# Kernel optimization log

Measured on AMD Instinct MI355X. Metric: run time of the kernel, lower is better.

Reference implementation:

```python
import jax, jax.numpy as jnp
import numpy as np

E = 8       # num_experts
TOP_K = 2
H = 512     # hidden_size
DFF = 2048  # expert FFN inner dim (4*H)
B, S = 4, 2048


def setup_inputs() -> dict:
    key = jax.random.key(0)
    k0, k1, k2, k3 = jax.random.split(key, 4)
    return {
        "hidden_states": jax.random.normal(k0, (B, S, H), jnp.float32),
        # router gate: kaiming-ish init scaled by 0.01 (near-uniform routing)
        "gate_w": jax.random.normal(k1, (E, H), jnp.float32) * 0.01,
        "w1": jax.random.normal(k2, (E, H, DFF), jnp.float32) * (1.0 / np.sqrt(H)),
        "b1": jnp.zeros((E, DFF), jnp.float32),
        "w2": jax.random.normal(k3, (E, DFF, H), jnp.float32) * (1.0 / np.sqrt(DFF)),
        "b2": jnp.zeros((E, H), jnp.float32),
    }


def reference(hidden_states, gate_w, w1, b1, w2, b2):
    # hidden_states: (B, S, H)
    b, s, h = hidden_states.shape
    flat = hidden_states.reshape(-1, h)                 # (T, H), T = B*S

    # --- TopKRouter (eval mode: no gaussian noise) ---
    logits = flat @ gate_w.T                            # (T, E)
    top_vals, top_idx = jax.lax.top_k(logits, TOP_K)    # (T, K)
    top_w = jax.nn.softmax(top_vals, axis=-1)           # softmax over selected k only

    # combine[t, e] = routing weight of expert e for token t (0 if not selected).
    # top_k indices are distinct per token, so summing over k matches the
    # original masked scatter-add output[mask] += weight * expert_out.
    combine = jnp.sum(
        jax.nn.one_hot(top_idx, E, dtype=flat.dtype) * top_w[..., None], axis=1
    )                                                   # (T, E)

    # --- experts: dense compute per expert, weighted combine ---
    out = jnp.zeros_like(flat)
    for e in range(E):  # fixed small loop over experts (not a data dim)
        hdn = jax.nn.gelu(flat @ w1[e] + b1[e])         # (T, DFF)
        out = out + combine[:, e:e + 1] * (hdn @ w2[e] + b2[e])
    return out.reshape(b, s, h)
```

## Files before the change

kernel.cpp:

```cpp
#include <hip/hip_runtime.h>
#include <hip/hip_bf16.h>

#define E_    8
#define H_    512
#define DFF_  2048
#define T_    8192
#define NSLOT (2 * T_)

typedef float  f32x4  __attribute__((ext_vector_type(4)));
typedef short  bf16x8 __attribute__((ext_vector_type(8)));

static __device__ __forceinline__ ushort f2bf(float f) {
  union { float f; unsigned u; } v; v.f = f;
  unsigned r = v.u + 0x7FFFu + ((v.u >> 16) & 1u);
  return (ushort)(r >> 16);
}

static __device__ __forceinline__ void gload16(const void* g, void* l) {
  __builtin_amdgcn_global_load_lds((const __attribute__((address_space(1))) void*)g,
                                   (__attribute__((address_space(3))) void*)l, 16, 0, 0);
}

__global__ void route_cast_kernel(const float* __restrict__ x, const float* __restrict__ gw,
                                  ushort* __restrict__ xb,
                                  float* __restrict__ slotw, int* __restrict__ slote) {
  int tokn = (blockIdx.x * blockDim.x + threadIdx.x) >> 6;
  int lane = threadIdx.x & 63;
  if (tokn >= T_) return;
  const float4* xr = (const float4*)(x + (size_t)tokn * H_ + lane * 8);
  float4 x0 = xr[0], x1 = xr[1];
  ushort v[8] = {f2bf(x0.x), f2bf(x0.y), f2bf(x0.z), f2bf(x0.w),
                 f2bf(x1.x), f2bf(x1.y), f2bf(x1.z), f2bf(x1.w)};
  *(uint4*)(xb + (size_t)tokn * H_ + lane * 8) = *(uint4*)v;

  float acc[E_];
#pragma unroll
  for (int e = 0; e < E_; ++e) {
    const float4* gr = (const float4*)(gw + e * H_ + lane * 8);
    float4 g0 = gr[0], g1 = gr[1];
    acc[e] = x0.x*g0.x + x0.y*g0.y + x0.z*g0.z + x0.w*g0.w
           + x1.x*g1.x + x1.y*g1.y + x1.z*g1.z + x1.w*g1.w;
  }
#pragma unroll
  for (int e = 0; e < E_; ++e) {
#pragma unroll
    for (int off = 32; off; off >>= 1)
      acc[e] += __shfl_xor(acc[e], off);
  }
  if (lane == 0) {
    float v1 = -1e30f, v2 = -1e30f; int i1 = 0, i2 = 0;
#pragma unroll
    for (int e = 0; e < E_; ++e) {
      float vv = acc[e];
      if (vv > v1)      { v2 = v1; i2 = i1; v1 = vv; i1 = e; }
      else if (vv > v2) { v2 = vv; i2 = e; }
    }
    float ex = expf(v2 - v1);
    float inv = 1.0f / (1.0f + ex);
    slote[2 * tokn] = i1;     slotw[2 * tokn] = inv;
    slote[2 * tokn + 1] = i2; slotw[2 * tokn + 1] = ex * inv;
  }
}

__global__ __launch_bounds__(1024) void listbuild_kernel(
    const int* __restrict__ slote, int* __restrict__ counts, int* __restrict__ lslot) {
  int tid = threadIdx.x, lane = tid & 63, wv = tid >> 6;
  int base = tid * 16;
  int myexp[16];
  unsigned char cnt[E_] = {0, 0, 0, 0, 0, 0, 0, 0};
#pragma unroll
  for (int i = 0; i < 16; ++i) {
    int e = slote[base + i];
    myexp[i] = e;
    cnt[e]++;
  }
  unsigned long long lo = 0, hi = 0;
#pragma unroll
  for (int e = 0; e < 4; ++e) {
    lo |= (unsigned long long)cnt[e] << (16 * e);
    hi |= (unsigned long long)cnt[e + 4] << (16 * e);
  }
  unsigned long long mylo = lo, myhi = hi;
#pragma unroll
  for (int off = 1; off < 64; off <<= 1) {
    unsigned long long tl = __shfl_up(lo, off);
    unsigned long long th = __shfl_up(hi, off);
    if (lane >= off) { lo += tl; hi += th; }
  }
  __shared__ unsigned long long wtotlo[16], wtothi[16];
  __shared__ unsigned long long wbaselo[16], wbasehi[16];
  if (lane == 63) { wtotlo[wv] = lo; wtothi[wv] = hi; }
  __syncthreads();
  if (tid == 0) {
    unsigned long long rl = 0, rh = 0;
#pragma unroll
    for (int w2 = 0; w2 < 16; ++w2) {
      wbaselo[w2] = rl; wbasehi[w2] = rh;
      rl += wtotlo[w2]; rh += wtothi[w2];
    }
#pragma unroll
    for (int e = 0; e < 4; ++e) {
      counts[e]     = (int)((rl >> (16 * e)) & 0xFFFF);
      counts[e + 4] = (int)((rh >> (16 * e)) & 0xFFFF);
    }
  }
  __syncthreads();
  unsigned long long exlo = wbaselo[wv] + lo - mylo;
  unsigned long long exhi = wbasehi[wv] + hi - myhi;
  int pos[E_];
#pragma unroll
  for (int e = 0; e < 4; ++e) {
    pos[e]     = (int)((exlo >> (16 * e)) & 0xFFFF);
    pos[e + 4] = (int)((exhi >> (16 * e)) & 0xFFFF);
  }
#pragma unroll
  for (int i = 0; i < 16; ++i) {
    int e = myexp[i];
    lslot[e * T_ + pos[e]] = base + i;
    pos[e]++;
  }
}

__global__ void transpose_cast_kernel(const float* __restrict__ in,
                                      ushort* __restrict__ out, int R, int C) {
  int e = blockIdx.z, r0 = blockIdx.y * 64, c0 = blockIdx.x * 64;
  __shared__ float tile[64][65];
  int t = threadIdx.x;
  int row = t >> 2, seg = t & 3;
  const float* src = in + ((size_t)e * R + r0 + row) * C + c0 + seg * 16;
#pragma unroll
  for (int i = 0; i < 4; ++i) {
    float4 v = *(const float4*)(src + i * 4);
    tile[row][seg * 16 + i * 4 + 0] = v.x;
    tile[row][seg * 16 + i * 4 + 1] = v.y;
    tile[row][seg * 16 + i * 4 + 2] = v.z;
    tile[row][seg * 16 + i * 4 + 3] = v.w;
  }
  __syncthreads();
  int c = t >> 2;
  ushort vals[16];
#pragma unroll
  for (int j = 0; j < 16; ++j) vals[j] = f2bf(tile[seg * 16 + j][c]);
  ushort* dst = out + ((size_t)e * C + c0 + c) * R + r0 + seg * 16;
  *(uint4*)(dst)     = *(uint4*)&vals[0];
  *(uint4*)(dst + 8) = *(uint4*)&vals[8];
}

__global__ __launch_bounds__(256, 2) void gemm1_kernel(
    const ushort* __restrict__ xb, const ushort* __restrict__ w1t,
    const float* __restrict__ b1, const int* __restrict__ counts,
    const int* __restrict__ lslot, ushort* __restrict__ hdn, int c0, int DC) {
  int e = blockIdx.z;
  int cnt = counts[e];
  int m0 = blockIdx.y * 128;
  if (m0 >= cnt) return;
  int n0 = c0 + blockIdx.x * 128;

  __shared__ ushort sA[128 * 64];
  __shared__ ushort sB[128 * 64];
  int tid = threadIdx.x, lane = tid & 63, wid = tid >> 6;
  int wm = wid >> 1, wn = wid & 1;
  const int* lst = lslot + e * T_;
  const ushort* w1e = w1t + (size_t)e * DFF_ * H_;

  int lrow = lane >> 3;
  int scol = ((lane & 7) ^ lrow) * 8;

  const ushort* asrc[4]; const ushort* bsrc[4];
#pragma unroll
  for (int is = 0; is < 4; ++is) {
    int row = (wid * 4 + is) * 8 + lrow;
    int r = m0 + row; if (r > cnt - 1) r = cnt - 1;
    asrc[is] = xb + (size_t)(lst[r] >> 1) * H_ + scol;
    bsrc[is] = w1e + (size_t)(n0 + row) * H_ + scol;
  }

  f32x4 acc[4][4];
#pragma unroll
  for (int i = 0; i < 4; ++i)
#pragma unroll
    for (int j = 0; j < 4; ++j) acc[i][j] = (f32x4){0.f, 0.f, 0.f, 0.f};

  for (int k0 = 0; k0 < H_; k0 += 64) {
    __syncthreads();
#pragma unroll
    for (int is = 0; is < 4; ++is) {
      gload16(asrc[is] + k0, &sA[(wid * 4 + is) * 512]);
      gload16(bsrc[is] + k0, &sB[(wid * 4 + is) * 512]);
    }
    __syncthreads();
#pragma unroll
    for (int s = 0; s < 2; ++s) {
      bf16x8 af[4], bfr[4];
#pragma unroll
      for (int i = 0; i < 4; ++i) {
        int row = wm * 64 + i * 16 + (lane & 15);
        af[i] = *(const bf16x8*)(&sA[row * 64 + (((s * 4 + (lane >> 4)) ^ (row & 7)) * 8)]);
      }
#pragma unroll
      for (int i = 0; i < 4; ++i) {
        int row = wn * 64 + i * 16 + (lane & 15);
        bfr[i] = *(const bf16x8*)(&sB[row * 64 + (((s * 4 + (lane >> 4)) ^ (row & 7)) * 8)]);
      }
#pragma unroll
      for (int i = 0; i < 4; ++i)
#pragma unroll
        for (int j = 0; j < 4; ++j)
          acc[i][j] = __builtin_amdgcn_mfma_f32_16x16x32_bf16(af[i], bfr[j], acc[i][j], 0, 0, 0);
    }
  }

  int cl = lane & 15, rg = lane >> 4;
  float b1v[4];
#pragma unroll
  for (int j = 0; j < 4; ++j) b1v[j] = b1[e * DFF_ + n0 + wn * 64 + j * 16 + cl];
#pragma unroll
  for (int i = 0; i < 4; ++i) {
    int rbase = m0 + wm * 64 + i * 16 + rg * 4;
#pragma unroll
    for (int r = 0; r < 4; ++r) {
      int gr = rbase + r;
      if (gr < cnt) {
        ushort* hrow = hdn + (size_t)lst[gr] * DC + (n0 - c0) + wn * 64 + cl;
#pragma unroll
        for (int j = 0; j < 4; ++j) {
          float v = acc[i][j][r] + b1v[j];
          float t = v + 0.044715f * v * v * v;
          float exv = __expf(1.5957691216057308f * t);
          float th = 1.0f - 2.0f / (exv + 1.0f);
          hrow[j * 16] = f2bf(0.5f * v * (1.0f + th));
        }
      }
    }
  }
}

__global__ __launch_bounds__(256, 2) void gemm2_kernel(
    const ushort* __restrict__ hdn, const ushort* __restrict__ w2t,
    const int* __restrict__ counts, const int* __restrict__ lslot,
    float* __restrict__ O2, int c0, int DC, int first) {
  int e = blockIdx.z;
  int cnt = counts[e];
  int m0 = blockIdx.y * 128;
  if (m0 >= cnt) return;
  int n0 = blockIdx.x * 128;

  __shared__ ushort sA[128 * 64];
  __shared__ ushort sB[128 * 64];
  int tid = threadIdx.x, lane = tid & 63, wid = tid >> 6;
  int wm = wid >> 1, wn = wid & 1;
  const int* lst = lslot + e * T_;
  const ushort* w2e = w2t + (size_t)e * H_ * DFF_ + c0;

  int lrow = lane >> 3;
  int scol = ((lane & 7) ^ lrow) * 8;

  const ushort* asrc[4]; const ushort* bsrc[4];
#pragma unroll
  for (int is = 0; is < 4; ++is) {
    int row = (wid * 4 + is) * 8 + lrow;
    int r = m0 + row; if (r > cnt - 1) r = cnt - 1;
    asrc[is] = hdn + (size_t)lst[r] * DC + scol;
    bsrc[is] = w2e + (size_t)(n0 + row) * DFF_ + scol;
  }

  f32x4 acc[4][4];
#pragma unroll
  for (int i = 0; i < 4; ++i)
#pragma unroll
    for (int j = 0; j < 4; ++j) acc[i][j] = (f32x4){0.f, 0.f, 0.f, 0.f};

  for (int k0 = 0; k0 < DC; k0 += 64) {
    __syncthreads();
#pragma unroll
    for (int is = 0; is < 4; ++is) {
      gload16(asrc[is] + k0, &sA[(wid * 4 + is) * 512]);
      gload16(bsrc[is] + k0, &sB[(wid * 4 + is) * 512]);
    }
    __syncthreads();
#pragma unroll
    for (int s = 0; s < 2; ++s) {
      bf16x8 af[4], bfr[4];
#pragma unroll
      for (int i = 0; i < 4; ++i) {
        int row = wm * 64 + i * 16 + (lane & 15);
        af[i] = *(const bf16x8*)(&sA[row * 64 + (((s * 4 + (lane >> 4)) ^ (row & 7)) * 8)]);
      }
#pragma unroll
      for (int i = 0; i < 4; ++i) {
        int row = wn * 64 + i * 16 + (lane & 15);
        bfr[i] = *(const bf16x8*)(&sB[row * 64 + (((s * 4 + (lane >> 4)) ^ (row & 7)) * 8)]);
      }
#pragma unroll
      for (int i = 0; i < 4; ++i)
#pragma unroll
        for (int j = 0; j < 4; ++j)
          acc[i][j] = __builtin_amdgcn_mfma_f32_16x16x32_bf16(af[i], bfr[j], acc[i][j], 0, 0, 0);
    }
  }

  int cl = lane & 15, rg = lane >> 4;
#pragma unroll
  for (int i = 0; i < 4; ++i) {
    int rbase = m0 + wm * 64 + i * 16 + rg * 4;
#pragma unroll
    for (int r = 0; r < 4; ++r) {
      int gr = rbase + r;
      if (gr < cnt) {
        float* orow = O2 + (size_t)lst[gr] * H_ + n0 + wn * 64 + cl;
        if (first) {
#pragma unroll
          for (int j = 0; j < 4; ++j) orow[j * 16] = acc[i][j][r];
        } else {
#pragma unroll
          for (int j = 0; j < 4; ++j) orow[j * 16] += acc[i][j][r];
        }
      }
    }
  }
}

__global__ void combine_kernel(const float* __restrict__ O2, const float* __restrict__ b2,
                               const float* __restrict__ slotw, const int* __restrict__ slote,
                               float* __restrict__ out) {
  int idx = blockIdx.x * 256 + threadIdx.x;
  int t = idx >> 7;
  int h4 = (idx & 127) * 4;
  int s0 = 2 * t, s1 = 2 * t + 1;
  float w0 = slotw[s0], w1 = slotw[s1];
  int e0 = slote[s0], e1 = slote[s1];
  float4 a = *(const float4*)(O2 + (size_t)s0 * H_ + h4);
  float4 b = *(const float4*)(O2 + (size_t)s1 * H_ + h4);
  float4 c = *(const float4*)(b2 + e0 * H_ + h4);
  float4 d = *(const float4*)(b2 + e1 * H_ + h4);
  float4 o;
  o.x = w0 * (a.x + c.x) + w1 * (b.x + d.x);
  o.y = w0 * (a.y + c.y) + w1 * (b.y + d.y);
  o.z = w0 * (a.z + c.z) + w1 * (b.z + d.z);
  o.w = w0 * (a.w + c.w) + w1 * (b.w + d.w);
  *(float4*)(out + (size_t)t * H_ + h4) = o;
}

extern "C" void kernel_launch(void* const* d_in, const int* in_sizes, int n_in,
                              void* d_out, int out_size, void* d_ws, size_t ws_size,
                              hipStream_t stream) {
  const float* x  = (const float*)d_in[0];
  const float* gw = (const float*)d_in[1];
  const float* w1 = (const float*)d_in[2];
  const float* b1 = (const float*)d_in[3];
  const float* w2 = (const float*)d_in[4];
  const float* b2 = (const float*)d_in[5];
  float* out = (float*)d_out;

  char* ws = (char*)d_ws;
  size_t off = 0;
  auto alloc = [&](size_t bytes) -> void* {
    void* p = ws + off; off += (bytes + 255) & ~(size_t)255; return p;
  };
  int*    counts = (int*)alloc(256);
  int*    lslot  = (int*)alloc((size_t)E_ * T_ * 4);
  float*  slotw  = (float*)alloc((size_t)NSLOT * 4);
  int*    slote  = (int*)alloc((size_t)NSLOT * 4);
  ushort* w1t    = (ushort*)alloc((size_t)E_ * DFF_ * H_ * 2);
  ushort* w2t    = (ushort*)alloc((size_t)E_ * H_ * DFF_ * 2);
  ushort* xb     = (ushort*)alloc((size_t)T_ * H_ * 2);
  float*  O2     = (float*)alloc((size_t)NSLOT * H_ * 4);

  int NC = 1;
  while (NC < 16 && off + (size_t)NSLOT * (DFF_ / NC) * 2 > ws_size) NC *= 2;
  int DC = DFF_ / NC;
  ushort* hdn = (ushort*)alloc((size_t)NSLOT * DC * 2);

  route_cast_kernel<<<T_ / 4, 256, 0, stream>>>(x, gw, xb, slotw, slote);
  listbuild_kernel<<<1, 1024, 0, stream>>>(slote, counts, lslot);
  transpose_cast_kernel<<<dim3(DFF_ / 64, H_ / 64, E_), 256, 0, stream>>>(w1, w1t, H_, DFF_);
  transpose_cast_kernel<<<dim3(H_ / 64, DFF_ / 64, E_), 256, 0, stream>>>(w2, w2t, DFF_, H_);

  for (int c = 0; c < NC; ++c) {
    gemm1_kernel<<<dim3(DC / 128, T_ / 128, E_), 256, 0, stream>>>(
        xb, w1t, b1, counts, lslot, hdn, c * DC, DC);
    gemm2_kernel<<<dim3(H_ / 128, T_ / 128, E_), 256, 0, stream>>>(
        hdn, w2t, counts, lslot, O2, c * DC, DC, c == 0);
  }
  combine_kernel<<<T_ * H_ / 1024, 256, 0, stream>>>(O2, b2, slotw, slote, out);
}
```

Baseline: 180.7 us.

## Double-buffer LDS tiles in expert GEMMs and fuse combine into gemm2 atomics

Both expert GEMM kernels now use two LDS buffers per operand. The next K tile is prefetched with global_load_lds while the current tile is multiplied, and the loop relies on explicit vmcnt waits and barriers. The separate combine kernel and the fp32 O2 slot buffer are removed: gemm2 scales its result by the routing weight, adds b2 on the last chunk, and atomically adds into the zeroed output. This saves a large intermediate write and read plus one launch, at the cost of atomic contention (two experts per token), a memset, and doubled LDS use that may lower occupancy.

```diff
diff --git a/kernel.cpp b/kernel.cpp
--- a/kernel.cpp
+++ b/kernel.cpp
@@ -156,8 +156,8 @@
   if (m0 >= cnt) return;
   int n0 = c0 + blockIdx.x * 128;
 
-  __shared__ ushort sA[128 * 64];
-  __shared__ ushort sB[128 * 64];
+  __shared__ ushort sA[2][128 * 64];
+  __shared__ ushort sB[2][128 * 64];
   int tid = threadIdx.x, lane = tid & 63, wid = tid >> 6;
   int wm = wid >> 1, wn = wid & 1;
   const int* lst = lslot + e * T_;
@@ -181,26 +181,39 @@
 #pragma unroll
     for (int j = 0; j < 4; ++j) acc[i][j] = (f32x4){0.f, 0.f, 0.f, 0.f};
 
-  for (int k0 = 0; k0 < H_; k0 += 64) {
-    __syncthreads();
-#pragma unroll
-    for (int is = 0; is < 4; ++is) {
-      gload16(asrc[is] + k0, &sA[(wid * 4 + is) * 512]);
-      gload16(bsrc[is] + k0, &sB[(wid * 4 + is) * 512]);
-    }
-    __syncthreads();
+#pragma unroll
+  for (int is = 0; is < 4; ++is) {
+    gload16(asrc[is], &sA[0][(wid * 4 + is) * 512]);
+    gload16(bsrc[is], &sB[0][(wid * 4 + is) * 512]);
+  }
+  int cur = 0;
+  const int NT = H_ / 64;
+  for (int t = 0; t < NT; ++t) {
+    if (t + 1 < NT) {
+      int k0 = (t + 1) * 64;
+#pragma unroll
+      for (int is = 0; is < 4; ++is) {
+        gload16(asrc[is] + k0, &sA[cur ^ 1][(wid * 4 + is) * 512]);
+        gload16(bsrc[is] + k0, &sB[cur ^ 1][(wid * 4 + is) * 512]);
+      }
+      asm volatile("s_waitcnt vmcnt(8)" ::: "memory");
+    } else {
+      asm volatile("s_waitcnt vmcnt(0)" ::: "memory");
+    }
+    __builtin_amdgcn_s_barrier();
+    asm volatile("" ::: "memory");
 #pragma unroll
     for (int s = 0; s < 2; ++s) {
       bf16x8 af[4], bfr[4];
 #pragma unroll
       for (int i = 0; i < 4; ++i) {
         int row = wm * 64 + i * 16 + (lane & 15);
-        af[i] = *(const bf16x8*)(&sA[row * 64 + (((s * 4 + (lane >> 4)) ^ (row & 7)) * 8)]);
+        af[i] = *(const bf16x8*)(&sA[cur][row * 64 + (((s * 4 + (lane >> 4)) ^ (row & 7)) * 8)]);
       }
 #pragma unroll
       for (int i = 0; i < 4; ++i) {
         int row = wn * 64 + i * 16 + (lane & 15);
-        bfr[i] = *(const bf16x8*)(&sB[row * 64 + (((s * 4 + (lane >> 4)) ^ (row & 7)) * 8)]);
+        bfr[i] = *(const bf16x8*)(&sB[cur][row * 64 + (((s * 4 + (lane >> 4)) ^ (row & 7)) * 8)]);
       }
 #pragma unroll
       for (int i = 0; i < 4; ++i)
@@ -208,6 +221,9 @@
         for (int j = 0; j < 4; ++j)
           acc[i][j] = __builtin_amdgcn_mfma_f32_16x16x32_bf16(af[i], bfr[j], acc[i][j], 0, 0, 0);
     }
+    asm volatile("" ::: "memory");
+    __builtin_amdgcn_s_barrier();
+    cur ^= 1;
   }
 
   int cl = lane & 15, rg = lane >> 4;
@@ -225,8 +241,8 @@
 #pragma unroll
         for (int j = 0; j < 4; ++j) {
           float v = acc[i][j][r] + b1v[j];
-          float t = v + 0.044715f * v * v * v;
-          float exv = __expf(1.5957691216057308f * t);
+          float t2 = v + 0.044715f * v * v * v;
+          float exv = __expf(1.5957691216057308f * t2);
           float th = 1.0f - 2.0f / (exv + 1.0f);
           hrow[j * 16] = f2bf(0.5f * v * (1.0f + th));
         }
@@ -237,16 +253,17 @@
 
 __global__ __launch_bounds__(256, 2) void gemm2_kernel(
     const ushort* __restrict__ hdn, const ushort* __restrict__ w2t,
+    const float* __restrict__ b2, const float* __restrict__ slotw,
     const int* __restrict__ counts, const int* __restrict__ lslot,
-    float* __restrict__ O2, int c0, int DC, int first) {
+    float* __restrict__ out, int c0, int DC, int addb) {
   int e = blockIdx.z;
   int cnt = counts[e];
   int m0 = blockIdx.y * 128;
   if (m0 >= cnt) return;
   int n0 = blockIdx.x * 128;
 
-  __shared__ ushort sA[128 * 64];
-  __shared__ ushort sB[128 * 64];
+  __shared__ ushort sA[2][128 * 64];
+  __shared__ ushort sB[2][128 * 64];
   int tid = threadIdx.x, lane = tid & 63, wid = tid >> 6;
   int wm = wid >> 1, wn = wid & 1;
   const int* lst = lslot + e * T_;
@@ -270,26 +287,41 @@
 #pragma unroll
     for (int j = 0; j < 4; ++j) acc[i][j] = (f32x4){0.f, 0.f, 0.f, 0.f};
 
-  for (int k0 = 0; k0 < DC; k0 += 64) {
-    __syncthreads();
-#pragma unroll
-    for (int is = 0; is < 4; ++is) {
-      gload16(asrc[is] + k0, &sA[(wid * 4 + is) * 512]);
-      gload16(bsrc[is] + k0, &sB[(wid * 4 + is) * 512]);
-    }
-    __syncthreads();
+#pragma unroll
+  for (int is = 0; is < 4; ++is) {
+    gload16(asrc[is], &sA[0][(wid * 4 + is) * 512]);
+    gload16(bsrc[is], &sB[0][(wid * 4 + is) * 512]);
+  }
+  int cur = 0;
+  const int NT = DFF_ / 64;
+  int nt = DC / 64;
+  (void)NT;
+  for (int t = 0; t < nt; ++t) {
+    if (t + 1 < nt) {
+      int k0 = (t + 1) * 64;
+#pragma unroll
+      for (int is = 0; is < 4; ++is) {
+        gload16(asrc[is] + k0, &sA[cur ^ 1][(wid * 4 + is) * 512]);
+        gload16(bsrc[is] + k0, &sB[cur ^ 1][(wid * 4 + is) * 512]);
+      }
+      asm volatile("s_waitcnt vmcnt(8)" ::: "memory");
+    } else {
+      asm volatile("s_waitcnt vmcnt(0)" ::: "memory");
+    }
+    __builtin_amdgcn_s_barrier();
+    asm volatile("" ::: "memory");
 #pragma unroll
     for (int s = 0; s < 2; ++s) {
       bf16x8 af[4], bfr[4];
 #pragma unroll
       for (int i = 0; i < 4; ++i) {
         int row = wm * 64 + i * 16 + (lane & 15);
-        af[i] = *(const bf16x8*)(&sA[row * 64 + (((s * 4 + (lane >> 4)) ^ (row & 7)) * 8)]);
+        af[i] = *(const bf16x8*)(&sA[cur][row * 64 + (((s * 4 + (lane >> 4)) ^ (row & 7)) * 8)]);
       }
 #pragma unroll
       for (int i = 0; i < 4; ++i) {
         int row = wn * 64 + i * 16 + (lane & 15);
-        bfr[i] = *(const bf16x8*)(&sB[row * 64 + (((s * 4 + (lane >> 4)) ^ (row & 7)) * 8)]);
+        bfr[i] = *(const bf16x8*)(&sB[cur][row * 64 + (((s * 4 + (lane >> 4)) ^ (row & 7)) * 8)]);
       }
 #pragma unroll
       for (int i = 0; i < 4; ++i)
@@ -297,9 +329,16 @@
         for (int j = 0; j < 4; ++j)
           acc[i][j] = __builtin_amdgcn_mfma_f32_16x16x32_bf16(af[i], bfr[j], acc[i][j], 0, 0, 0);
     }
+    asm volatile("" ::: "memory");
+    __builtin_amdgcn_s_barrier();
+    cur ^= 1;
   }
 
   int cl = lane & 15, rg = lane >> 4;
+  float b2v[4];
+#pragma unroll
+  for (int j = 0; j < 4; ++j)
+    b2v[j] = addb ? b2[e * H_ + n0 + wn * 64 + j * 16 + cl] : 0.0f;
 #pragma unroll
   for (int i = 0; i < 4; ++i) {
     int rbase = m0 + wm * 64 + i * 16 + rg * 4;
@@ -307,38 +346,15 @@
     for (int r = 0; r < 4; ++r) {
       int gr = rbase + r;
       if (gr < cnt) {
-        float* orow = O2 + (size_t)lst[gr] * H_ + n0 + wn * 64 + cl;
-        if (first) {
-#pragma unroll
-          for (int j = 0; j < 4; ++j) orow[j * 16] = acc[i][j][r];
-        } else {
-#pragma unroll
-          for (int j = 0; j < 4; ++j) orow[j * 16] += acc[i][j][r];
-        }
-      }
-    }
-  }
-}
-
-__global__ void combine_kernel(const float* __restrict__ O2, const float* __restrict__ b2,
-                               const float* __restrict__ slotw, const int* __restrict__ slote,
-                               float* __restrict__ out) {
-  int idx = blockIdx.x * 256 + threadIdx.x;
-  int t = idx >> 7;
-  int h4 = (idx & 127) * 4;
-  int s0 = 2 * t, s1 = 2 * t + 1;
-  float w0 = slotw[s0], w1 = slotw[s1];
-  int e0 = slote[s0], e1 = slote[s1];
-  float4 a = *(const float4*)(O2 + (size_t)s0 * H_ + h4);
-  float4 b = *(const float4*)(O2 + (size_t)s1 * H_ + h4);
-  float4 c = *(const float4*)(b2 + e0 * H_ + h4);
-  float4 d = *(const float4*)(b2 + e1 * H_ + h4);
-  float4 o;
-  o.x = w0 * (a.x + c.x) + w1 * (b.x + d.x);
-  o.y = w0 * (a.y + c.y) + w1 * (b.y + d.y);
-  o.z = w0 * (a.z + c.z) + w1 * (b.z + d.z);
-  o.w = w0 * (a.w + c.w) + w1 * (b.w + d.w);
-  *(float4*)(out + (size_t)t * H_ + h4) = o;
+        int slot = lst[gr];
+        float wgt = slotw[slot];
+        float* orow = out + (size_t)(slot >> 1) * H_ + n0 + wn * 64 + cl;
+#pragma unroll
+        for (int j = 0; j < 4; ++j)
+          atomicAdd(&orow[j * 16], wgt * (acc[i][j][r] + b2v[j]));
+      }
+    }
+  }
 }
 
 extern "C" void kernel_launch(void* const* d_in, const int* in_sizes, int n_in,
@@ -364,13 +380,13 @@
   ushort* w1t    = (ushort*)alloc((size_t)E_ * DFF_ * H_ * 2);
   ushort* w2t    = (ushort*)alloc((size_t)E_ * H_ * DFF_ * 2);
   ushort* xb     = (ushort*)alloc((size_t)T_ * H_ * 2);
-  float*  O2     = (float*)alloc((size_t)NSLOT * H_ * 4);
 
   int NC = 1;
   while (NC < 16 && off + (size_t)NSLOT * (DFF_ / NC) * 2 > ws_size) NC *= 2;
   int DC = DFF_ / NC;
   ushort* hdn = (ushort*)alloc((size_t)NSLOT * DC * 2);
 
+  hipMemsetAsync(out, 0, (size_t)out_size * sizeof(float), stream);
   route_cast_kernel<<<T_ / 4, 256, 0, stream>>>(x, gw, xb, slotw, slote);
   listbuild_kernel<<<1, 1024, 0, stream>>>(slote, counts, lslot);
   transpose_cast_kernel<<<dim3(DFF_ / 64, H_ / 64, E_), 256, 0, stream>>>(w1, w1t, H_, DFF_);
@@ -380,7 +396,6 @@
     gemm1_kernel<<<dim3(DC / 128, T_ / 128, E_), 256, 0, stream>>>(
         xb, w1t, b1, counts, lslot, hdn, c * DC, DC);
     gemm2_kernel<<<dim3(H_ / 128, T_ / 128, E_), 256, 0, stream>>>(
-        hdn, w2t, counts, lslot, O2, c * DC, DC, c == 0);
-  }
-  combine_kernel<<<T_ * H_ / 1024, 256, 0, stream>>>(O2, b2, slotw, slote, out);
-}
+        hdn, w2t, b2, slotw, counts, lslot, out, c * DC, DC, c == NC - 1);
+  }
+}
```

After: 219.0 us. 1.21x slower.

## Fuse weighted combine into gemm2 via atomics and interleave experts in grid

Applied to the files above, without the earlier changes.

Removes the separate combine kernel and the per-slot O2 fp32 buffer. gemm2 now scales its partial results by the routing weight, adds the bias on the last chunk, and atomically accumulates into the zeroed output. Block indices are flattened so the expert is the fastest-varying index, which spreads early-exiting blocks across experts. This trades O2 writes and reads plus a kernel launch for float atomic traffic, an output memset, and nondeterministic summation order.

```diff
diff --git a/kernel.cpp b/kernel.cpp
--- a/kernel.cpp
+++ b/kernel.cpp
@@ -150,11 +150,15 @@
     const ushort* __restrict__ xb, const ushort* __restrict__ w1t,
     const float* __restrict__ b1, const int* __restrict__ counts,
     const int* __restrict__ lslot, ushort* __restrict__ hdn, int c0, int DC) {
-  int e = blockIdx.z;
+  int bid = blockIdx.x;
+  int e = bid & (E_ - 1);
+  int nx = DC / 128;
+  int bx = (bid >> 3) % nx;
+  int by = (bid >> 3) / nx;
   int cnt = counts[e];
-  int m0 = blockIdx.y * 128;
+  int m0 = by * 128;
   if (m0 >= cnt) return;
-  int n0 = c0 + blockIdx.x * 128;
+  int n0 = c0 + bx * 128;
 
   __shared__ ushort sA[128 * 64];
   __shared__ ushort sB[128 * 64];
@@ -225,8 +229,8 @@
 #pragma unroll
         for (int j = 0; j < 4; ++j) {
           float v = acc[i][j][r] + b1v[j];
-          float t = v + 0.044715f * v * v * v;
-          float exv = __expf(1.5957691216057308f * t);
+          float t2 = v + 0.044715f * v * v * v;
+          float exv = __expf(1.5957691216057308f * t2);
           float th = 1.0f - 2.0f / (exv + 1.0f);
           hrow[j * 16] = f2bf(0.5f * v * (1.0f + th));
         }
@@ -237,13 +241,18 @@
 
 __global__ __launch_bounds__(256, 2) void gemm2_kernel(
     const ushort* __restrict__ hdn, const ushort* __restrict__ w2t,
+    const float* __restrict__ b2, const float* __restrict__ slotw,
     const int* __restrict__ counts, const int* __restrict__ lslot,
-    float* __restrict__ O2, int c0, int DC, int first) {
-  int e = blockIdx.z;
+    float* __restrict__ out, int c0, int DC, int addb) {
+  int bid = blockIdx.x;
+  int e = bid & (E_ - 1);
+  const int nx = H_ / 128;
+  int bx = (bid >> 3) % nx;
+  int by = (bid >> 3) / nx;
   int cnt = counts[e];
-  int m0 = blockIdx.y * 128;
+  int m0 = by * 128;
   if (m0 >= cnt) return;
-  int n0 = blockIdx.x * 128;
+  int n0 = bx * 128;
 
   __shared__ ushort sA[128 * 64];
   __shared__ ushort sB[128 * 64];
@@ -300,6 +309,10 @@
   }
 
   int cl = lane & 15, rg = lane >> 4;
+  float b2v[4];
+#pragma unroll
+  for (int j = 0; j < 4; ++j)
+    b2v[j] = addb ? b2[e * H_ + n0 + wn * 64 + j * 16 + cl] : 0.0f;
 #pragma unroll
   for (int i = 0; i < 4; ++i) {
     int rbase = m0 + wm * 64 + i * 16 + rg * 4;
@@ -307,38 +320,15 @@
     for (int r = 0; r < 4; ++r) {
       int gr = rbase + r;
       if (gr < cnt) {
-        float* orow = O2 + (size_t)lst[gr] * H_ + n0 + wn * 64 + cl;
-        if (first) {
-#pragma unroll
-          for (int j = 0; j < 4; ++j) orow[j * 16] = acc[i][j][r];
-        } else {
-#pragma unroll
-          for (int j = 0; j < 4; ++j) orow[j * 16] += acc[i][j][r];
-        }
-      }
-    }
-  }
-}
-
-__global__ void combine_kernel(const float* __restrict__ O2, const float* __restrict__ b2,
-                               const float* __restrict__ slotw, const int* __restrict__ slote,
-                               float* __restrict__ out) {
-  int idx = blockIdx.x * 256 + threadIdx.x;
-  int t = idx >> 7;
-  int h4 = (idx & 127) * 4;
-  int s0 = 2 * t, s1 = 2 * t + 1;
-  float w0 = slotw[s0], w1 = slotw[s1];
-  int e0 = slote[s0], e1 = slote[s1];
-  float4 a = *(const float4*)(O2 + (size_t)s0 * H_ + h4);
-  float4 b = *(const float4*)(O2 + (size_t)s1 * H_ + h4);
-  float4 c = *(const float4*)(b2 + e0 * H_ + h4);
-  float4 d = *(const float4*)(b2 + e1 * H_ + h4);
-  float4 o;
-  o.x = w0 * (a.x + c.x) + w1 * (b.x + d.x);
-  o.y = w0 * (a.y + c.y) + w1 * (b.y + d.y);
-  o.z = w0 * (a.z + c.z) + w1 * (b.z + d.z);
-  o.w = w0 * (a.w + c.w) + w1 * (b.w + d.w);
-  *(float4*)(out + (size_t)t * H_ + h4) = o;
+        int slot = lst[gr];
+        float wgt = slotw[slot];
+        float* orow = out + (size_t)(slot >> 1) * H_ + n0 + wn * 64 + cl;
+#pragma unroll
+        for (int j = 0; j < 4; ++j)
+          atomicAdd(&orow[j * 16], wgt * (acc[i][j][r] + b2v[j]));
+      }
+    }
+  }
 }
 
 extern "C" void kernel_launch(void* const* d_in, const int* in_sizes, int n_in,
@@ -364,23 +354,22 @@
   ushort* w1t    = (ushort*)alloc((size_t)E_ * DFF_ * H_ * 2);
   ushort* w2t    = (ushort*)alloc((size_t)E_ * H_ * DFF_ * 2);
   ushort* xb     = (ushort*)alloc((size_t)T_ * H_ * 2);
-  float*  O2     = (float*)alloc((size_t)NSLOT * H_ * 4);
 
   int NC = 1;
   while (NC < 16 && off + (size_t)NSLOT * (DFF_ / NC) * 2 > ws_size) NC *= 2;
   int DC = DFF_ / NC;
   ushort* hdn = (ushort*)alloc((size_t)NSLOT * DC * 2);
 
+  hipMemsetAsync(out, 0, (size_t)out_size * sizeof(float), stream);
   route_cast_kernel<<<T_ / 4, 256, 0, stream>>>(x, gw, xb, slotw, slote);
   listbuild_kernel<<<1, 1024, 0, stream>>>(slote, counts, lslot);
   transpose_cast_kernel<<<dim3(DFF_ / 64, H_ / 64, E_), 256, 0, stream>>>(w1, w1t, H_, DFF_);
   transpose_cast_kernel<<<dim3(H_ / 64, DFF_ / 64, E_), 256, 0, stream>>>(w2, w2t, DFF_, H_);
 
   for (int c = 0; c < NC; ++c) {
-    gemm1_kernel<<<dim3(DC / 128, T_ / 128, E_), 256, 0, stream>>>(
+    gemm1_kernel<<<E_ * (DC / 128) * (T_ / 128), 256, 0, stream>>>(
         xb, w1t, b1, counts, lslot, hdn, c * DC, DC);
-    gemm2_kernel<<<dim3(H_ / 128, T_ / 128, E_), 256, 0, stream>>>(
-        hdn, w2t, counts, lslot, O2, c * DC, DC, c == 0);
-  }
-  combine_kernel<<<T_ * H_ / 1024, 256, 0, stream>>>(O2, b2, slotw, slote, out);
-}
+    gemm2_kernel<<<E_ * (H_ / 128) * (T_ / 128), 256, 0, stream>>>(
+        hdn, w2t, b2, slotw, counts, lslot, out, c * DC, DC, c == NC - 1);
+  }
+}
```

Measured after the change: 171.0 us. -5.3%, faster.
